# Kernel optimization log

Measured on AMD Instinct MI355X. Metric: run time of the kernel, lower is better.

The kernel has to match this reference:

```python
import jax, jax.numpy as jnp
import numpy as np

HEADS = 12
DIM = 768


def setup_inputs() -> dict:
    key = jax.random.key(0)
    ks = jax.random.split(key, 11)
    B, T, D, H = 2, 2048, DIM, HEADS
    s = 0.02
    inp = {
        "x": jax.random.normal(ks[0], (B, T, D), dtype=jnp.float32),
        "Wq": jax.random.normal(ks[1], (D, D), dtype=jnp.float32) * s,
        "bq": jax.random.normal(ks[2], (D,), dtype=jnp.float32) * s,
        "Wk": jax.random.normal(ks[3], (D, D), dtype=jnp.float32) * s,
        "bk": jax.random.normal(ks[4], (D,), dtype=jnp.float32) * s,
        "Wv": jax.random.normal(ks[5], (D, D), dtype=jnp.float32) * s,
        "bv": jax.random.normal(ks[6], (D,), dtype=jnp.float32) * s,
        # shaped-attention affine params (torch init: alpha=1, beta=0, gamma=0;
        # perturb so all terms are exercised)
        "alpha": jnp.ones((1, H, 1, 1), jnp.float32) + 0.1 * jax.random.normal(ks[7], (1, H, 1, 1)),
        "beta": 0.1 * jax.random.normal(ks[8], (1, H, 1, 1), dtype=jnp.float32),
        "gamma": 0.1 * jax.random.normal(ks[9], (1, H, 1, 1), dtype=jnp.float32),
        # registered buffer C (zeros in the source)
        "C": jnp.zeros((H, 1, 1), jnp.float32),
    }
    return inp


def reference(x, Wq, bq, Wk, bk, Wv, bv, alpha, beta, gamma, C):
    B, T, D = x.shape
    H = HEADS
    hd = D // H
    scale = hd ** -0.5
    # torch nn.Linear: y = x @ W.T + b ; then [B,T,H,hd] -> [B,H,T,hd]
    q = (x @ Wq.T + bq).reshape(B, T, H, hd).transpose(0, 2, 1, 3)
    k = (x @ Wk.T + bk).reshape(B, T, H, hd).transpose(0, 2, 1, 3)
    v = (x @ Wv.T + bv).reshape(B, T, H, hd).transpose(0, 2, 1, 3)
    attn = jax.nn.softmax(jnp.einsum("bhqd,bhkd->bhqk", q, k) * scale, axis=-1)
    # shaped correction: alpha*I + beta*softmax - gamma*C
    eye = jnp.eye(T, dtype=x.dtype)
    attn = alpha * eye + beta * attn - gamma * C  # C:(H,1,1) broadcasts over T,T
    out = jnp.einsum("bhqk,bhkd->bhqd", attn, v)
    return out.transpose(0, 2, 1, 3).reshape(B, T, D)
```

## Files before the change

kernel.cpp:

```cpp
#include <hip/hip_runtime.h>
#include <hip/hip_bf16.h>

#define HEADS 12
#define HD 64
#define DMODEL 768
#define TSEQ 2048
#define BATCH 2
#define NTOK (BATCH*TSEQ)
#define NQKV (3*DMODEL)
#define KSPLIT 4
#define BK 64
#define KVBLK 64
#define QSCALE 0.1803368801f

typedef __attribute__((ext_vector_type(8))) short bf16x8;
typedef __attribute__((ext_vector_type(4))) short bf16x4;
typedef __attribute__((ext_vector_type(4))) float f32x4;
typedef __attribute__((ext_vector_type(16))) float f32x16;
typedef __attribute__((ext_vector_type(2))) unsigned uint32x2;

static __device__ inline float bf2f(short s) {
  union { float f; unsigned u; } cv; cv.u = ((unsigned)(unsigned short)s) << 16; return cv.f;
}
static __device__ inline short f2bf(float f) {
  union { float f; unsigned u; } cv; cv.f = f;
  unsigned u = cv.u;
  unsigned r = u + 0x7FFF + ((u >> 16) & 1);
  return (short)(r >> 16);
}

__global__ void cvt_kernel(const float* __restrict__ x,
                           const float* __restrict__ Wq, const float* __restrict__ Wk,
                           const float* __restrict__ Wv,
                           const float* __restrict__ bq, const float* __restrict__ bk,
                           const float* __restrict__ bv,
                           short* __restrict__ Xb, short* __restrict__ Wc,
                           float* __restrict__ bc) {
  const int NX4 = NTOK*DMODEL/4;
  const int WSZ = DMODEL*DMODEL;
  const int NW4 = 3*WSZ/4;
  const int total = NX4 + NW4 + NQKV;
  for (int i = blockIdx.x*blockDim.x + threadIdx.x; i < total; i += gridDim.x*blockDim.x) {
    if (i < NX4) {
      f32x4 v = *(const f32x4*)&x[i*4];
      bf16x4 o;
      #pragma unroll
      for (int j=0;j<4;j++) o[j] = f2bf(v[j]);
      *(bf16x4*)&Xb[i*4] = o;
    } else if (i < NX4 + NW4) {
      int j = (i - NX4)*4;
      const float* src = (j < WSZ) ? &Wq[j] : (j < 2*WSZ) ? &Wk[j - WSZ] : &Wv[j - 2*WSZ];
      f32x4 v = *(const f32x4*)src;
      bf16x4 o;
      #pragma unroll
      for (int jj=0;jj<4;jj++) o[jj] = f2bf(v[jj]);
      *(bf16x4*)&Wc[j] = o;
    } else {
      int o = i - NX4 - NW4;
      bc[o] = (o < DMODEL) ? bq[o] : (o < 2*DMODEL) ? bk[o - DMODEL] : bv[o - 2*DMODEL];
    }
  }
}

__global__ __launch_bounds__(256,3) void qkv_gemm(const short* __restrict__ Xb,
                                                  const short* __restrict__ Wc,
                                                  const float* __restrict__ bc,
                                                  short* __restrict__ Q, short* __restrict__ K,
                                                  short* __restrict__ V, short* __restrict__ Vt,
                                                  float* __restrict__ vs) {
  __shared__ __align__(16) char lds[49152];
  const int nbn = NQKV/64;
  int swzb = ((blockIdx.x & 7) * 144) + (blockIdx.x >> 3);
  int bm = swzb / nbn, bn = swzb % nbn;
  int trow = bm*128, tcol = bn*64;
  int tid = threadIdx.x;
  int w = tid >> 6, l = tid & 63;
  int wr = w >> 1, wc = w & 1;
  int lr = l & 15, lg = l >> 4;

  int rbase = tid >> 3;
  int csw   = (tid & 7) ^ (rbase & 7);
  const short* pA = Xb + (size_t)(trow + rbase)*DMODEL + csw*8;
  const short* pB = Wc + (size_t)(tcol + rbase)*DMODEL + csw*8;

  unsigned aoff[4][2], boff[2][2];
  #pragma unroll
  for (int m=0;m<4;m++)
    #pragma unroll
    for (int kc2=0;kc2<2;kc2++) {
      int rowa = wr*64 + m*16 + lr;
      aoff[m][kc2] = rowa*128 + (((kc2*4+lg) ^ (rowa&7))*16);
    }
  #pragma unroll
  for (int n=0;n<2;n++)
    #pragma unroll
    for (int kc2=0;kc2<2;kc2++) {
      int rowb = wc*32 + n*16 + lr;
      boff[n][kc2] = rowb*128 + (((kc2*4+lg) ^ (rowb&7))*16);
    }

  f32x4 acc[4][2];
  #pragma unroll
  for (int m=0;m<4;m++)
    #pragma unroll
    for (int n=0;n<2;n++) acc[m][n] = (f32x4)0.f;

  auto stage = [&](int buf, int ks) {
    int k0 = ks*BK;
    unsigned base = (unsigned)buf*24576u;
    #pragma unroll
    for (int i=0;i<4;i++)
      __builtin_amdgcn_global_load_lds(
        (const __attribute__((address_space(1))) unsigned int*)(pA + k0 + i*(32*DMODEL)),
        (__attribute__((address_space(3))) unsigned int*)(lds + base + (i*256 + w*64)*16),
        16, 0, 0);
    #pragma unroll
    for (int i=0;i<2;i++)
      __builtin_amdgcn_global_load_lds(
        (const __attribute__((address_space(1))) unsigned int*)(pB + k0 + i*(32*DMODEL)),
        (__attribute__((address_space(3))) unsigned int*)(lds + base + 16384 + (i*256 + w*64)*16),
        16, 0, 0);
  };

  stage(0, 0);
  asm volatile("s_waitcnt vmcnt(0)");
  __syncthreads();

  const int NKS = DMODEL/BK;
  for (int ks = 0; ks < NKS; ks++) {
    int cur = ks & 1;
    if (ks + 1 < NKS) stage(cur ^ 1, ks + 1);
    unsigned abase = (unsigned)cur*24576u, bbase = abase + 16384u;
    bf16x8 af[4][2], bfr[2][2];
    #pragma unroll
    for (int m=0;m<4;m++)
      #pragma unroll
      for (int kc2=0;kc2<2;kc2++)
        af[m][kc2] = *(const bf16x8*)(lds + abase + aoff[m][kc2]);
    #pragma unroll
    for (int n=0;n<2;n++)
      #pragma unroll
      for (int kc2=0;kc2<2;kc2++)
        bfr[n][kc2] = *(const bf16x8*)(lds + bbase + boff[n][kc2]);
    __builtin_amdgcn_s_setprio(1);
    #pragma unroll
    for (int m=0;m<4;m++)
      #pragma unroll
      for (int n=0;n<2;n++)
        #pragma unroll
        for (int kc2=0;kc2<2;kc2++)
          acc[m][n] = __builtin_amdgcn_mfma_f32_16x16x32_bf16(af[m][kc2], bfr[n][kc2], acc[m][n], 0, 0, 0);
    __builtin_amdgcn_s_setprio(0);
    __syncthreads();
  }

  short* ltile = (short*)lds;
  int sel = tcol / DMODEL;
  int hh  = (tcol % DMODEL) >> 6;
  float qsc = (sel == 0) ? QSCALE : 1.f;
  float bcv[2];
  #pragma unroll
  for (int n=0;n<2;n++) bcv[n] = bc[tcol + wc*32 + n*16 + lr];
  #pragma unroll
  for (int m=0;m<4;m++)
    #pragma unroll
    for (int n=0;n<2;n++)
      #pragma unroll
      for (int j=0;j<4;j++)
        ltile[(wr*64 + m*16 + lg*4 + j)*64 + wc*32 + n*16 + lr] = f2bf((acc[m][n][j] + bcv[n]) * qsc);
  __syncthreads();

  short* dstQKV = (sel == 0) ? Q : (sel == 1) ? K : V;
  int b = trow >> 11;
  #pragma unroll
  for (int rr=0; rr<4; rr++) {
    int idx = rr*256 + tid;
    int r2 = idx >> 3, c2 = idx & 7;
    int tt = (trow + r2) & (TSEQ-1);
    bf16x8 val = *(const bf16x8*)&ltile[r2*64 + c2*8];
    *(bf16x8*)&dstQKV[((size_t)(b*HEADS + hh)*TSEQ + tt)*HD + c2*8] = val;
  }
  if (sel == 2) {
    #pragma unroll
    for (int rr=0; rr<4; rr++) {
      int idx = rr*256 + tid;
      int col = idx >> 4, tc8 = idx & 15;
      int tt0 = (trow + tc8*8) & (TSEQ-1);
      bf16x8 v;
      #pragma unroll
      for (int j=0;j<8;j++) v[j] = ltile[(tc8*8 + j)*64 + col];
      *(bf16x8*)&Vt[((size_t)(b*HEADS + hh)*HD + col)*TSEQ + tt0] = v;
    }
    int col = tid & 63;
    int rh  = tid >> 6;
    float s = 0.f;
    #pragma unroll
    for (int i=0;i<32;i++) s += bf2f(ltile[(rh*32 + i)*64 + col]);
    atomicAdd(&vs[(b*HEADS + hh)*HD + col], s);
  }
}

__global__ __launch_bounds__(256,3) void attn_kernel(
    const short* __restrict__ Q, const short* __restrict__ K,
    const short* __restrict__ Vt,
    short* __restrict__ po, float* __restrict__ pml) {
  const int nqt = TSEQ/128;
  int bid = blockIdx.x;
  int ks_id = bid % KSPLIT;
  int r = bid / KSPLIT;
  int qt = r % nqt;
  int bh = r / nqt;

  int tid = threadIdx.x;
  int w = tid >> 6, lane = tid & 63;
  int q5 = lane & 31, hi = lane >> 5;
  int qrow = qt*128 + w*32 + q5;

  __shared__ __align__(16) char kbuf[2][8192];
  __shared__ __align__(16) char vbuf[2][8192];

  const short* Qp  = Q  + (size_t)bh*TSEQ*HD;
  const short* Kp  = K  + (size_t)bh*TSEQ*HD;
  const short* Vtp = Vt + (size_t)bh*HD*TSEQ;

  bf16x8 qf[4];
  #pragma unroll
  for (int c=0;c<4;c++)
    qf[c] = *(const bf16x8*)&Qp[(size_t)qrow*HD + c*16 + hi*8];

  const int ksoff = ks_id*(TSEQ/KSPLIT);

  auto stage = [&](int buf, int kt) {
    int kb = ksoff + kt*KVBLK;
    #pragma unroll
    for (int i=0;i<2;i++) {
      int l0 = i*256 + w*64;
      int l  = l0 + lane;
      int rr = l >> 3, cc = l & 7;
      int sk = cc ^ (rr & 7);
      __builtin_amdgcn_global_load_lds(
        (const __attribute__((address_space(1))) unsigned int*)(Kp + (size_t)(kb + rr)*HD + sk*8),
        (__attribute__((address_space(3))) unsigned int*)(kbuf[buf] + l0*16),
        16, 0, 0);
      __builtin_amdgcn_global_load_lds(
        (const __attribute__((address_space(1))) unsigned int*)(Vtp + (size_t)rr*TSEQ + kb + sk*8),
        (__attribute__((address_space(3))) unsigned int*)(vbuf[buf] + l0*16),
        16, 0, 0);
    }
  };

  f32x16 o0 = (f32x16)0.f, o1 = (f32x16)0.f;
  float psum0 = 0.f, psum1 = 0.f;
  const int rx = q5 & 7;

  stage(0, 0);
  asm volatile("s_waitcnt vmcnt(0)");
  __syncthreads();

  const int NT = TSEQ/KSPLIT/KVBLK;
  for (int kt = 0; kt < NT; kt++) {
    int cur = kt & 1;
    if (kt + 1 < NT) stage(cur ^ 1, kt + 1);

    #pragma unroll
    for (int t=0;t<2;t++) {
      bf16x8 kf[4];
      #pragma unroll
      for (int c=0;c<4;c++)
        kf[c] = *(const bf16x8*)(kbuf[cur] + (t*32+q5)*128 + (((c*2+hi) ^ rx)*16));

      f32x16 st = (f32x16)0.f;
      __builtin_amdgcn_s_setprio(1);
      #pragma unroll
      for (int c=0;c<4;c++)
        st = __builtin_amdgcn_mfma_f32_32x32x16_bf16(kf[c], qf[c], st, 0, 0, 0);
      __builtin_amdgcn_s_setprio(0);

      bf16x8 vf0[2], vf1[2];
      #pragma unroll
      for (int ks2=0;ks2<2;ks2++) {
        int kc = ((t*4 + ks2*2 + hi) ^ rx)*16;
        vf0[ks2] = *(const bf16x8*)(vbuf[cur] + q5*128 + kc);
        vf1[ks2] = *(const bf16x8*)(vbuf[cur] + (q5+32)*128 + kc);
      }

      #pragma unroll
      for (int i=0;i<16;i+=2) {
        st[i]   = __builtin_amdgcn_exp2f(st[i]);
        st[i+1] = __builtin_amdgcn_exp2f(st[i+1]);
        psum0 += st[i];
        psum1 += st[i+1];
      }
      unsigned pw[4][2];
      #pragma unroll
      for (int a=0;a<4;a++)
        #pragma unroll
        for (int p=0;p<2;p++) {
          union { __hip_bfloat162 h; unsigned u; } cvp;
          cvp.h = __float22bfloat162_rn(float2{st[a*4+2*p], st[a*4+2*p+1]});
          pw[a][p] = cvp.u;
        }
      #pragma unroll
      for (int ks2=0;ks2<2;ks2++) {
        uint32x2 s0 = __builtin_amdgcn_permlane32_swap(pw[2*ks2][0],   pw[2*ks2][0],   false, false);
        uint32x2 s1 = __builtin_amdgcn_permlane32_swap(pw[2*ks2][1],   pw[2*ks2][1],   false, false);
        uint32x2 s2 = __builtin_amdgcn_permlane32_swap(pw[2*ks2+1][0], pw[2*ks2+1][0], false, false);
        uint32x2 s3 = __builtin_amdgcn_permlane32_swap(pw[2*ks2+1][1], pw[2*ks2+1][1], false, false);
        union { unsigned u[4]; bf16x8 v; } bw;
        bw.u[0] = s0[0];
        bw.u[1] = s1[0];
        bw.u[2] = s2[1];
        bw.u[3] = s3[1];
        __builtin_amdgcn_s_setprio(1);
        o0 = __builtin_amdgcn_mfma_f32_32x32x16_bf16(vf0[ks2], bw.v, o0, 0, 0, 0);
        o1 = __builtin_amdgcn_mfma_f32_32x32x16_bf16(vf1[ks2], bw.v, o1, 0, 0, 0);
        __builtin_amdgcn_s_setprio(0);
      }
    }

    asm volatile("s_waitcnt vmcnt(0)");
    __syncthreads();
  }

  float psum = psum0 + psum1;
  float ltot = psum + __shfl_xor(psum, 32);
  size_t gq = (size_t)bh*TSEQ + qrow;
  if (!hi) pml[gq*KSPLIT + ks_id] = ltot;

  #pragma unroll
  for (int rg=0; rg<4; rg++) {
    bf16x4 pk0, pk1;
    #pragma unroll
    for (int rj=0;rj<4;rj++) { pk0[rj] = f2bf(o0[rg*4+rj]); pk1[rj] = f2bf(o1[rg*4+rj]); }
    int d0 = rg*8 + hi*4;
    *(bf16x4*)&po[(gq*KSPLIT + ks_id)*HD + d0]      = pk0;
    *(bf16x4*)&po[(gq*KSPLIT + ks_id)*HD + 32 + d0] = pk1;
  }
}

__global__ __launch_bounds__(256) void combine_kernel(
    const short* __restrict__ po, const float* __restrict__ pml,
    const short* __restrict__ V, const float* __restrict__ vs,
    const float* __restrict__ alpha, const float* __restrict__ beta,
    const float* __restrict__ gamma, const float* __restrict__ Cc,
    float* __restrict__ out) {
  int t = threadIdx.x;
  size_t gq = (size_t)blockIdx.x*32 + (t >> 3);
  int d0 = (t & 7)*8;
  int bh = (int)(gq >> 11), q = (int)(gq & (TSEQ-1));
  int b = bh / HEADS, h = bh % HEADS;

  float L = 0.f;
  float acc[8] = {0,0,0,0,0,0,0,0};
  #pragma unroll
  for (int i=0;i<KSPLIT;i++) {
    L += pml[gq*KSPLIT + i];
    bf16x8 p8 = *(const bf16x8*)&po[(gq*KSPLIT + i)*HD + d0];
    #pragma unroll
    for (int j=0;j<8;j++) acc[j] += bf2f(p8[j]);
  }
  float inv = 1.f / L;
  float al = alpha[h], be = beta[h], gc = gamma[h]*Cc[h];
  bf16x8 v8 = *(const bf16x8*)&V[((size_t)bh*TSEQ + q)*HD + d0];
  f32x4 vs0 = *(const f32x4*)&vs[bh*HD + d0];
  f32x4 vs1 = *(const f32x4*)&vs[bh*HD + d0 + 4];
  f32x4 r0, r1;
  #pragma unroll
  for (int j=0;j<4;j++) {
    r0[j] = al*bf2f(v8[j])   + be*acc[j]*inv   - gc*vs0[j];
    r1[j] = al*bf2f(v8[j+4]) + be*acc[j+4]*inv - gc*vs1[j];
  }
  float* op = &out[((size_t)b*TSEQ + q)*DMODEL + h*HD + d0];
  *(f32x4*)op = r0;
  *(f32x4*)(op+4) = r1;
}

extern "C" void kernel_launch(void* const* d_in, const int* in_sizes, int n_in,
                              void* d_out, int out_size, void* d_ws, size_t ws_size,
                              hipStream_t stream) {
  const float* x     = (const float*)d_in[0];
  const float* Wq    = (const float*)d_in[1];
  const float* bq    = (const float*)d_in[2];
  const float* Wk    = (const float*)d_in[3];
  const float* bk    = (const float*)d_in[4];
  const float* Wv    = (const float*)d_in[5];
  const float* bv    = (const float*)d_in[6];
  const float* alpha = (const float*)d_in[7];
  const float* beta  = (const float*)d_in[8];
  const float* gamma = (const float*)d_in[9];
  const float* Cc    = (const float*)d_in[10];
  float* out = (float*)d_out;

  char* ws = (char*)d_ws;
  size_t off = 0;
  auto alloc = [&](size_t bytes) -> void* {
    void* p = ws + off; off += (bytes + 255) & ~(size_t)255; return p;
  };
  short* Xb = (short*)alloc((size_t)NTOK*DMODEL*2);
  short* Wc = (short*)alloc((size_t)NQKV*DMODEL*2);
  float* bc = (float*)alloc((size_t)NQKV*4);
  short* Q  = (short*)alloc((size_t)BATCH*HEADS*TSEQ*HD*2);
  short* K  = (short*)alloc((size_t)BATCH*HEADS*TSEQ*HD*2);
  short* V  = (short*)alloc((size_t)BATCH*HEADS*TSEQ*HD*2);
  short* Vt = (short*)alloc((size_t)BATCH*HEADS*TSEQ*HD*2);
  float* vs = (float*)alloc((size_t)BATCH*HEADS*HD*4);
  short* po  = (short*)alloc((size_t)BATCH*HEADS*TSEQ*KSPLIT*HD*2);
  float* pml = (float*)alloc((size_t)BATCH*HEADS*TSEQ*KSPLIT*4);

  hipMemsetAsync(vs, 0, (size_t)BATCH*HEADS*HD*4, stream);
  cvt_kernel<<<1024, 256, 0, stream>>>(x, Wq, Wk, Wv, bq, bk, bv, Xb, Wc, bc);
  qkv_gemm<<<(NTOK/128)*(NQKV/64), 256, 0, stream>>>(Xb, Wc, bc, Q, K, V, Vt, vs);
  attn_kernel<<<BATCH*HEADS*(TSEQ/128)*KSPLIT, 256, 0, stream>>>(Q, K, Vt, po, pml);
  combine_kernel<<<BATCH*HEADS*TSEQ/32, 256, 0, stream>>>(po, pml, V, vs, alpha, beta, gamma, Cc, out);
}
```

Before: 90.60 us.

## Fold vs memset into cvt kernel, raise attn occupancy, defer V loads

```diff
diff --git a/kernel.cpp b/kernel.cpp
--- a/kernel.cpp
+++ b/kernel.cpp
@@ -35,12 +35,14 @@
                            const float* __restrict__ bq, const float* __restrict__ bk,
                            const float* __restrict__ bv,
                            short* __restrict__ Xb, short* __restrict__ Wc,
-                           float* __restrict__ bc) {
+                           float* __restrict__ bc, float* __restrict__ vs) {
+  int g = blockIdx.x*blockDim.x + threadIdx.x;
+  if (g < BATCH*HEADS*HD) vs[g] = 0.f;
   const int NX4 = NTOK*DMODEL/4;
   const int WSZ = DMODEL*DMODEL;
   const int NW4 = 3*WSZ/4;
   const int total = NX4 + NW4 + NQKV;
-  for (int i = blockIdx.x*blockDim.x + threadIdx.x; i < total; i += gridDim.x*blockDim.x) {
+  for (int i = g; i < total; i += gridDim.x*blockDim.x) {
     if (i < NX4) {
       f32x4 v = *(const f32x4*)&x[i*4];
       bf16x4 o;
@@ -123,7 +125,7 @@
   };
 
   stage(0, 0);
-  asm volatile("s_waitcnt vmcnt(0)");
+  asm volatile("s_waitcnt vmcnt(0)" ::: "memory");
   __syncthreads();
 
   const int NKS = DMODEL/BK;
@@ -200,7 +202,7 @@
   }
 }
 
-__global__ __launch_bounds__(256,3) void attn_kernel(
+__global__ __launch_bounds__(256,4) void attn_kernel(
     const short* __restrict__ Q, const short* __restrict__ K,
     const short* __restrict__ Vt,
     short* __restrict__ po, float* __restrict__ pml) {
@@ -254,8 +256,8 @@
   const int rx = q5 & 7;
 
   stage(0, 0);
-  asm volatile("s_waitcnt vmcnt(0)");
-  __syncthreads();
+  asm volatile("s_waitcnt vmcnt(0)" ::: "memory");
+  __builtin_amdgcn_s_barrier();
 
   const int NT = TSEQ/KSPLIT/KVBLK;
   for (int kt = 0; kt < NT; kt++) {
@@ -275,14 +277,6 @@
       for (int c=0;c<4;c++)
         st = __builtin_amdgcn_mfma_f32_32x32x16_bf16(kf[c], qf[c], st, 0, 0, 0);
       __builtin_amdgcn_s_setprio(0);
-
-      bf16x8 vf0[2], vf1[2];
-      #pragma unroll
-      for (int ks2=0;ks2<2;ks2++) {
-        int kc = ((t*4 + ks2*2 + hi) ^ rx)*16;
-        vf0[ks2] = *(const bf16x8*)(vbuf[cur] + q5*128 + kc);
-        vf1[ks2] = *(const bf16x8*)(vbuf[cur] + (q5+32)*128 + kc);
-      }
 
       #pragma unroll
       for (int i=0;i<16;i+=2) {
@@ -311,15 +305,20 @@
         bw.u[1] = s1[0];
         bw.u[2] = s2[1];
         bw.u[3] = s3[1];
+        int kc = ((t*4 + ks2*2 + hi) ^ rx)*16;
+        bf16x8 vf0 = *(const bf16x8*)(vbuf[cur] + q5*128 + kc);
+        bf16x8 vf1 = *(const bf16x8*)(vbuf[cur] + (q5+32)*128 + kc);
         __builtin_amdgcn_s_setprio(1);
-        o0 = __builtin_amdgcn_mfma_f32_32x32x16_bf16(vf0[ks2], bw.v, o0, 0, 0, 0);
-        o1 = __builtin_amdgcn_mfma_f32_32x32x16_bf16(vf1[ks2], bw.v, o1, 0, 0, 0);
+        o0 = __builtin_amdgcn_mfma_f32_32x32x16_bf16(vf0, bw.v, o0, 0, 0, 0);
+        o1 = __builtin_amdgcn_mfma_f32_32x32x16_bf16(vf1, bw.v, o1, 0, 0, 0);
         __builtin_amdgcn_s_setprio(0);
       }
     }
 
-    asm volatile("s_waitcnt vmcnt(0)");
-    __syncthreads();
+    if (kt + 1 < NT) {
+      asm volatile("s_waitcnt vmcnt(0)" ::: "memory");
+      __builtin_amdgcn_s_barrier();
+    }
   }
 
   float psum = psum0 + psum1;
@@ -407,8 +406,7 @@
   short* po  = (short*)alloc((size_t)BATCH*HEADS*TSEQ*KSPLIT*HD*2);
   float* pml = (float*)alloc((size_t)BATCH*HEADS*TSEQ*KSPLIT*4);
 
-  hipMemsetAsync(vs, 0, (size_t)BATCH*HEADS*HD*4, stream);
-  cvt_kernel<<<1024, 256, 0, stream>>>(x, Wq, Wk, Wv, bq, bk, bv, Xb, Wc, bc);
+  cvt_kernel<<<2048, 256, 0, stream>>>(x, Wq, Wk, Wv, bq, bk, bv, Xb, Wc, bc, vs);
   qkv_gemm<<<(NTOK/128)*(NQKV/64), 256, 0, stream>>>(Xb, Wc, bc, Q, K, V, Vt, vs);
   attn_kernel<<<BATCH*HEADS*(TSEQ/128)*KSPLIT, 256, 0, stream>>>(Q, K, Vt, po, pml);
   combine_kernel<<<BATCH*HEADS*TSEQ/32, 256, 0, stream>>>(po, pml, V, vs, alpha, beta, gamma, Cc, out);
```

New measurement: 85.13 us. 6.0% less time.
